# Kernel tuning notes

Measured on AMD Instinct MI355X. Metric: run time of the kernel, lower is better.

The kernel has to match this reference:

```python
import jax, jax.numpy as jnp
import numpy as np

N, FEATS, CLASSES, E = 100000, 32, 16, 1600000
EMB_DIM = 1 + int(np.log2(FEATS))  # 6
HIDDEN = 3 + EMB_DIM               # 9
DEPTH = 10
DIFF = 0.9


def setup_inputs() -> dict:
    key = jax.random.key(0)
    ks = jax.random.split(key, 10)
    s = lambda k, *sh: jax.random.normal(k, sh, dtype=jnp.float32)
    return {
        "x": s(ks[0], N, FEATS),
        "edges": jax.random.randint(ks[1], (2, E), 0, N, dtype=jnp.int64),
        "emb_table": s(ks[2], FEATS, EMB_DIM) * 0.1,
        "W1": s(ks[3], 1 + EMB_DIM, HIDDEN) * 0.3,
        "b1": jnp.zeros((HIDDEN,), jnp.float32),
        "W2": s(ks[4], HIDDEN, 1) * 0.3,
        "b2": jnp.zeros((1,), jnp.float32),
        "Wout": s(ks[5], FEATS, CLASSES) * 0.1,
        "bout": jnp.zeros((CLASSES,), jnp.float32),
    }


def reference(x, edges, emb_table, W1, b1, W2, b2, Wout, bout):
    n, f = x.shape
    src, dst = edges[0], edges[1]
    # symmetric degree normalization (parameter-free GraphConv)
    deg = jax.ops.segment_sum(jnp.ones((src.shape[0],), x.dtype), dst, num_segments=n)
    deg = jnp.maximum(deg, 1.0)
    norm = jax.lax.rsqrt(deg[src] * deg[dst])  # [E]

    def conv(h):
        return jax.ops.segment_sum(h[src] * norm[:, None], dst, num_segments=n)

    def diffuse(h):
        h0 = h
        for _ in range(DEPTH):
            h = conv(h) * DIFF + (1.0 - DIFF) * h0
        return h

    x = diffuse(x)
    # per-(node, class) MLP: x.t().reshape(-1,1) orders rows class-major
    col = x.T.reshape(-1, 1)                       # [f*n, 1]
    emb = jnp.repeat(emb_table, n, axis=0)         # [f*n, EMB_DIM] (class cl repeated n times)
    h = jnp.concatenate([col, emb], axis=1)        # [f*n, 1+EMB_DIM]
    h = jax.nn.relu(h @ W1 + b1)
    h = h @ W2 + b2                                # [f*n, 1]
    x = h.reshape(f, n).T                          # [n, f]
    x = diffuse(x)
    return x @ Wout + bout
```

## Files before the change

kernel.cpp:

```cpp
#include <hip/hip_runtime.h>
#include <hip/hip_fp16.h>

#define ELL_CAP 64
#define NSLICE 8
#define EPB 2048


__global__ __launch_bounds__(256) void ell_fill(
    const int* __restrict__ edges, int* __restrict__ deg,
    int* __restrict__ ell, int e, int n, int slice_sz) {
    int slice = blockIdx.x & (NSLICE - 1);
    int chunk = blockIdx.x >> 3;
    int lo = slice * slice_sz;
    int hi = min(n, lo + slice_sz);
    int base = chunk * EPB + threadIdx.x;
    int d[EPB / 256], s[EPB / 256];
#pragma unroll
    for (int k = 0; k < EPB / 256; ++k) {
        int i = base + k * 256;
        int valid = i < e;
        int ii = valid ? i : 0;
        int dv = edges[e + ii];
        int sv = edges[ii];
        d[k] = valid ? dv : -1;
        s[k] = sv;
    }
#pragma unroll
    for (int k = 0; k < EPB / 256; ++k) {
        int dv = d[k];
        if (dv < lo || dv >= hi) continue;
        int slot = atomicAdd(&deg[dv], 1);
        if (slot < ELL_CAP) ell[((size_t)dv << 6) + slot] = s[k];
    }
}

__global__ void nodeconst_kernel(const int* __restrict__ deg, float* __restrict__ rs,
                                 float* __restrict__ sq, float* __restrict__ wdeg,
                                 int* __restrict__ ell, int n) {
    int i = blockIdx.x * blockDim.x + threadIdx.x;
    if (i > n) return;
    int v = (i < n) ? deg[i] : 0;
    float d = (float)max(v, 1);
    float r = rsqrtf(d);
    rs[i] = r;
    sq[i] = sqrtf(d);
    wdeg[i] = 0.9f * r * r;
    if (i < n) {
        int dg = min(v, ELL_CAP);
        int dgp = (dg + 7) & ~7;
        for (int k = dg; k < dgp; ++k) ell[((size_t)i << 6) + k] = n;
    }
}

__global__ void prescale_kernel(const float2* __restrict__ x2, const float* __restrict__ rs,
                                __half2* __restrict__ g, int n) {
    int i = blockIdx.x * blockDim.x + threadIdx.x;
    int node = i >> 4;
    if (node > n) return;
    if (node == n) { g[i] = __floats2half2_rn(0.f, 0.f); return; }
    float2 v = x2[i];
    float r = rs[node];
    g[i] = __floats2half2_rn(v.x * r, v.y * r);
}


union H4 {
    uint2 u;
    __half2 h[2];
};

__device__ __forceinline__ void issue8(H4 (&P)[8], int idx, const uint2* __restrict__ gin, int q) {
    int t[8];
#pragma unroll
    for (int l = 0; l < 8; ++l) t[l] = __shfl(idx, l, 8);
#pragma unroll
    for (int l = 0; l < 8; ++l) P[l].u = gin[(size_t)t[l] * 8 + q];
}

__device__ __forceinline__ void accum8(H4 (&P)[8], __half2& b0l, __half2& b0h,
                                       __half2& b1l, __half2& b1h,
                                       __half2& b2l, __half2& b2h,
                                       __half2& b3l, __half2& b3h) {
    b0l = __hadd2(b0l, P[0].h[0]); b0h = __hadd2(b0h, P[0].h[1]);
    b1l = __hadd2(b1l, P[1].h[0]); b1h = __hadd2(b1h, P[1].h[1]);
    b2l = __hadd2(b2l, P[2].h[0]); b2h = __hadd2(b2h, P[2].h[1]);
    b3l = __hadd2(b3l, P[3].h[0]); b3h = __hadd2(b3h, P[3].h[1]);
    b0l = __hadd2(b0l, P[4].h[0]); b0h = __hadd2(b0h, P[4].h[1]);
    b1l = __hadd2(b1l, P[5].h[0]); b1h = __hadd2(b1h, P[5].h[1]);
    b2l = __hadd2(b2l, P[6].h[0]); b2h = __hadd2(b2h, P[6].h[1]);
    b3l = __hadd2(b3l, P[7].h[0]); b3h = __hadd2(b3h, P[7].h[1]);
}

__global__ __launch_bounds__(256) void conv_kernel(
    const uint2* __restrict__ gin, const uint2* __restrict__ g0,
    uint2* __restrict__ gout, const int* __restrict__ deg,
    const int* __restrict__ ell, const float* __restrict__ wdeg, int n) {
    int gid = blockIdx.x * blockDim.x + threadIdx.x;
    int node = gid >> 3;
    int q = gid & 7;
    if (node > n) return;
    int dg = (node < n) ? min(deg[node], ELL_CAP) : 0;
    int trips = (dg + 7) >> 3;
    int j0 = node << 6;
    float w = wdeg[node];
    H4 g0v;
    g0v.u = g0[gid];
    float ax = 0.f, ay = 0.f, az = 0.f, aw = 0.f;
    __half2 b0l = __floats2half2_rn(0.f, 0.f), b0h = b0l;
    __half2 b1l = b0l, b1h = b0l;
    __half2 b2l = b0l, b2h = b0l;
    __half2 b3l = b0l, b3h = b0l;

    auto ldidx = [&](int r) -> int {
        int v = ell[j0 + (min(r, 7) << 3) + q];
        return (r < trips) ? v : n;
    };

    if (trips > 0) {
        H4 A[8], B[8];
        int ia = ldidx(0);
        int ib = ldidx(1);
        issue8(A, ia, gin, q);
        issue8(B, ib, gin, q);
        int iters = (trips + 1) >> 1;
        for (int t = 0; t < iters; ++t) {
            int na = ldidx(2 * t + 2);
            int nb = ldidx(2 * t + 3);
            accum8(A, b0l, b0h, b1l, b1h, b2l, b2h, b3l, b3h);
            issue8(A, na, gin, q);
            accum8(B, b0l, b0h, b1l, b1h, b2l, b2h, b3l, b3h);
            issue8(B, nb, gin, q);
            {
                float2 ft;
                ft = __half22float2(b0l); ax += ft.x; ay += ft.y;
                ft = __half22float2(b0h); az += ft.x; aw += ft.y;
                ft = __half22float2(b1l); ax += ft.x; ay += ft.y;
                ft = __half22float2(b1h); az += ft.x; aw += ft.y;
                ft = __half22float2(b2l); ax += ft.x; ay += ft.y;
                ft = __half22float2(b2h); az += ft.x; aw += ft.y;
                ft = __half22float2(b3l); ax += ft.x; ay += ft.y;
                ft = __half22float2(b3h); az += ft.x; aw += ft.y;
                b0l = __floats2half2_rn(0.f, 0.f); b0h = b0l;
                b1l = b0l; b1h = b0l;
                b2l = b0l; b2h = b0l;
                b3l = b0l; b3h = b0l;
            }
        }
    }

    float2 g0lo = __half22float2(g0v.h[0]);
    float2 g0hi = __half22float2(g0v.h[1]);
    float rx = w * ax + 0.1f * g0lo.x;
    float ry = w * ay + 0.1f * g0lo.y;
    float rz = w * az + 0.1f * g0hi.x;
    float rw = w * aw + 0.1f * g0hi.y;
    H4 o;
    o.h[0] = __floats2half2_rn(rx, ry);
    o.h[1] = __floats2half2_rn(rz, rw);
    gout[gid] = o.u;
}


__global__ __launch_bounds__(256) void mlp_kernel(
    const __half* __restrict__ gin, __half* __restrict__ gout,
    const float* __restrict__ rs, const float* __restrict__ sq,
    const float* __restrict__ emb,
    const float* __restrict__ W1,
    const float* __restrict__ b1,
    const float* __restrict__ W2,
    const float* __restrict__ b2,
    int n) {
    __shared__ float c[32][9];
    __shared__ float w0[9], w2[9];
    __shared__ float b2s;
    int tid = threadIdx.x;
    for (int i = tid; i < 288; i += blockDim.x) {
        int f = i / 9, jj = i % 9;
        float acc = b1[jj];
#pragma unroll
        for (int k = 0; k < 6; ++k) acc += emb[f * 6 + k] * W1[(1 + k) * 9 + jj];
        c[f][jj] = acc;
    }
    if (tid < 9) { w0[tid] = W1[tid]; w2[tid] = W2[tid]; }
    if (tid == 0) b2s = b2[0];
    __syncthreads();
    int gid = blockIdx.x * blockDim.x + tid;
    int node = gid >> 5;
    if (node > n) return;
    if (node == n) { gout[gid] = __float2half_rn(0.f); return; }
    int f = gid & 31;
    float xv = __half2float(gin[gid]) * sq[node];
    float acc = b2s;
#pragma unroll
    for (int jj = 0; jj < 9; ++jj)
        acc += fmaxf(xv * w0[jj] + c[f][jj], 0.0f) * w2[jj];
    gout[gid] = __float2half_rn(acc * rs[node]);
}


__global__ __launch_bounds__(256) void out_kernel(
    const __half* __restrict__ g, const float* __restrict__ sq,
    const float* __restrict__ Wout, const float* __restrict__ bout,
    float* __restrict__ out, int n) {
    __shared__ float w[32 * 16];
    __shared__ float bo[16];
    int tid = threadIdx.x;
    for (int i = tid; i < 512; i += blockDim.x) w[i] = Wout[i];
    if (tid < 16) bo[tid] = bout[tid];
    __syncthreads();
    int gid = blockIdx.x * blockDim.x + tid;
    int node = gid >> 4;
    int cls = gid & 15;
    if (node >= n) return;
    const __half* gr = g + (size_t)node * 32;
    float acc = 0.0f;
#pragma unroll
    for (int f = 0; f < 32; ++f) acc += __half2float(gr[f]) * w[f * 16 + cls];
    out[gid] = acc * sq[node] + bo[cls];
}

extern "C" void kernel_launch(void* const* d_in, const int* in_sizes, int n_in,
                              void* d_out, int out_size, void* d_ws, size_t ws_size,
                              hipStream_t stream) {
    const float* x    = (const float*)d_in[0];
    const int* edges  = (const int*)d_in[1];
    const float* emb  = (const float*)d_in[2];
    const float* W1   = (const float*)d_in[3];
    const float* b1   = (const float*)d_in[4];
    const float* W2   = (const float*)d_in[5];
    const float* b2   = (const float*)d_in[6];
    const float* Wout = (const float*)d_in[7];
    const float* bout = (const float*)d_in[8];
    float* out        = (float*)d_out;

    const int N = in_sizes[0] / 32;
    const int E = in_sizes[1] / 2;

    size_t off = 0;
    auto walloc = [&](size_t bytes) {
        void* p = (char*)d_ws + off;
        off += (bytes + 255) & ~(size_t)255;
        return p;
    };
    int*     deg   = (int*)    walloc((size_t)(N + 1) * 4);
    float*   rs    = (float*)  walloc((size_t)(N + 1) * 4);
    float*   sq    = (float*)  walloc((size_t)(N + 1) * 4);
    float*   wdeg  = (float*)  walloc((size_t)(N + 1) * 4);
    int*     ell   = (int*)    walloc((size_t)(N + 1) * ELL_CAP * 4 + 256);
    __half*  g0buf = (__half*) walloc((size_t)(N + 1) * 32 * 2);
    __half*  bufA  = (__half*) walloc((size_t)(N + 1) * 32 * 2);
    __half*  bufB  = (__half*) walloc((size_t)(N + 1) * 32 * 2);

    hipMemsetAsync(deg, 0, (size_t)(N + 1) * 4, stream);
    {
        int slice_sz = (N + NSLICE - 1) / NSLICE;
        int chunks = (E + EPB - 1) / EPB;
        ell_fill<<<chunks * NSLICE, 256, 0, stream>>>(edges, deg, ell, E, N, slice_sz);
    }
    nodeconst_kernel<<<(N + 1 + 255) / 256, 256, 0, stream>>>(deg, rs, sq, wdeg, ell, N);

    const int conv_blocks = ((N + 1) * 8 + 255) / 256;
    const int elem_blocks = ((N + 1) * 32 + 255) / 256;
    const int pair_blocks = ((N + 1) * 16 + 255) / 256;

    prescale_kernel<<<pair_blocks, 256, 0, stream>>>((const float2*)x, rs,
                                                     (__half2*)g0buf, N);

    {
        const uint2* gin = (const uint2*)g0buf;
        for (int it = 0; it < 10; ++it) {
            uint2* go = (uint2*)((it & 1) ? bufB : bufA);
            conv_kernel<<<conv_blocks, 256, 0, stream>>>(gin, (const uint2*)g0buf, go,
                                                         deg, ell, wdeg, N);
            gin = go;
        }
    }
    mlp_kernel<<<elem_blocks, 256, 0, stream>>>(bufB, g0buf, rs, sq, emb, W1, b1, W2, b2, N);

    {
        const uint2* gin = (const uint2*)g0buf;
        for (int it = 0; it < 10; ++it) {
            uint2* go = (uint2*)((it & 1) ? bufB : bufA);
            conv_kernel<<<conv_blocks, 256, 0, stream>>>(gin, (const uint2*)g0buf, go,
                                                         deg, ell, wdeg, N);
            gin = go;
        }
    }
    out_kernel<<<(N * 16 + 255) / 256, 256, 0, stream>>>(bufB, sq, Wout, bout, out, N);
}
```

Measured before the change: 618.7 us.

## Split feature buffers into two 16-channel halves and run conv per half

Stores the 32-feature fp16 node state as two separate 16-feature planes and launches the ELL gather conv twice per diffusion step, once per plane, with 4 lanes per node. Each plane is half as large, so the gathered working set is more likely to stay resident in L2/MALL during the random neighbor gathers. The cost is twice the kernel launches, reading the ELL index lists twice, and narrower per-node gathers.

Result: slower. 829.3 us (+34.1%).

```diff
diff --git a/kernel.cpp b/kernel.cpp
--- a/kernel.cpp
+++ b/kernel.cpp
@@ -53,14 +53,21 @@
 }
 
 __global__ void prescale_kernel(const float2* __restrict__ x2, const float* __restrict__ rs,
-                                __half2* __restrict__ g, int n) {
+                                __half2* __restrict__ glo, __half2* __restrict__ ghi, int n) {
     int i = blockIdx.x * blockDim.x + threadIdx.x;
     int node = i >> 4;
     if (node > n) return;
-    if (node == n) { g[i] = __floats2half2_rn(0.f, 0.f); return; }
-    float2 v = x2[i];
-    float r = rs[node];
-    g[i] = __floats2half2_rn(v.x * r, v.y * r);
+    int p = i & 15;
+    __half2 v;
+    if (node == n) {
+        v = __floats2half2_rn(0.f, 0.f);
+    } else {
+        float2 t = x2[i];
+        float r = rs[node];
+        v = __floats2half2_rn(t.x * r, t.y * r);
+    }
+    if (p < 8) glo[(size_t)node * 8 + p] = v;
+    else       ghi[(size_t)node * 8 + (p - 8)] = v;
 }
 
 
@@ -69,12 +76,13 @@
     __half2 h[2];
 };
 
-__device__ __forceinline__ void issue8(H4 (&P)[8], int idx, const uint2* __restrict__ gin, int q) {
-    int t[8];
-#pragma unroll
-    for (int l = 0; l < 8; ++l) t[l] = __shfl(idx, l, 8);
-#pragma unroll
-    for (int l = 0; l < 8; ++l) P[l].u = gin[(size_t)t[l] * 8 + q];
+__device__ __forceinline__ void issue8h(H4 (&P)[8], int i0, int i1,
+                                        const uint2* __restrict__ gin, int q) {
+#pragma unroll
+    for (int j = 0; j < 8; ++j) {
+        int s = __shfl((j & 1) ? i1 : i0, j >> 1, 4);
+        P[j].u = gin[(size_t)s * 4 + q];
+    }
 }
 
 __device__ __forceinline__ void accum8(H4 (&P)[8], __half2& b0l, __half2& b0h,
@@ -91,13 +99,13 @@
     b3l = __hadd2(b3l, P[7].h[0]); b3h = __hadd2(b3h, P[7].h[1]);
 }
 
-__global__ __launch_bounds__(256) void conv_kernel(
+__global__ __launch_bounds__(256) void conv_half(
     const uint2* __restrict__ gin, const uint2* __restrict__ g0,
     uint2* __restrict__ gout, const int* __restrict__ deg,
     const int* __restrict__ ell, const float* __restrict__ wdeg, int n) {
     int gid = blockIdx.x * blockDim.x + threadIdx.x;
-    int node = gid >> 3;
-    int q = gid & 7;
+    int node = gid >> 2;
+    int q = gid & 3;
     if (node > n) return;
     int dg = (node < n) ? min(deg[node], ELL_CAP) : 0;
     int trips = (dg + 7) >> 3;
@@ -111,25 +119,30 @@
     __half2 b2l = b0l, b2h = b0l;
     __half2 b3l = b0l, b3h = b0l;
 
-    auto ldidx = [&](int r) -> int {
-        int v = ell[j0 + (min(r, 7) << 3) + q];
-        return (r < trips) ? v : n;
+    auto ldidx2 = [&](int r, int& i0, int& i1) {
+        int rr = min(r, 7);
+        int v0 = ell[j0 + (rr << 3) + 2 * q];
+        int v1 = ell[j0 + (rr << 3) + 2 * q + 1];
+        i0 = (r < trips) ? v0 : n;
+        i1 = (r < trips) ? v1 : n;
     };
 
     if (trips > 0) {
         H4 A[8], B[8];
-        int ia = ldidx(0);
-        int ib = ldidx(1);
-        issue8(A, ia, gin, q);
-        issue8(B, ib, gin, q);
+        int ia0, ia1, ib0, ib1;
+        ldidx2(0, ia0, ia1);
+        ldidx2(1, ib0, ib1);
+        issue8h(A, ia0, ia1, gin, q);
+        issue8h(B, ib0, ib1, gin, q);
         int iters = (trips + 1) >> 1;
         for (int t = 0; t < iters; ++t) {
-            int na = ldidx(2 * t + 2);
-            int nb = ldidx(2 * t + 3);
+            int na0, na1, nb0, nb1;
+            ldidx2(2 * t + 2, na0, na1);
+            ldidx2(2 * t + 3, nb0, nb1);
             accum8(A, b0l, b0h, b1l, b1h, b2l, b2h, b3l, b3h);
-            issue8(A, na, gin, q);
+            issue8h(A, na0, na1, gin, q);
             accum8(B, b0l, b0h, b1l, b1h, b2l, b2h, b3l, b3h);
-            issue8(B, nb, gin, q);
+            issue8h(B, nb0, nb1, gin, q);
             {
                 float2 ft;
                 ft = __half22float2(b0l); ax += ft.x; ay += ft.y;
@@ -162,7 +175,8 @@
 
 
 __global__ __launch_bounds__(256) void mlp_kernel(
-    const __half* __restrict__ gin, __half* __restrict__ gout,
+    const __half* __restrict__ ginlo, const __half* __restrict__ ginhi,
+    __half* __restrict__ goutlo, __half* __restrict__ gouthi,
     const float* __restrict__ rs, const float* __restrict__ sq,
     const float* __restrict__ emb,
     const float* __restrict__ W1,
@@ -187,19 +201,23 @@
     int gid = blockIdx.x * blockDim.x + tid;
     int node = gid >> 5;
     if (node > n) return;
-    if (node == n) { gout[gid] = __float2half_rn(0.f); return; }
     int f = gid & 31;
-    float xv = __half2float(gin[gid]) * sq[node];
+    size_t half_idx = (size_t)node * 16 + (f & 15);
+    __half* dst = (f < 16) ? (goutlo + half_idx) : (gouthi + half_idx);
+    if (node == n) { *dst = __float2half_rn(0.f); return; }
+    const __half* src = (f < 16) ? (ginlo + half_idx) : (ginhi + half_idx);
+    float xv = __half2float(*src) * sq[node];
     float acc = b2s;
 #pragma unroll
     for (int jj = 0; jj < 9; ++jj)
         acc += fmaxf(xv * w0[jj] + c[f][jj], 0.0f) * w2[jj];
-    gout[gid] = __float2half_rn(acc * rs[node]);
+    *dst = __float2half_rn(acc * rs[node]);
 }
 
 
 __global__ __launch_bounds__(256) void out_kernel(
-    const __half* __restrict__ g, const float* __restrict__ sq,
+    const __half* __restrict__ glo, const __half* __restrict__ ghi,
+    const float* __restrict__ sq,
     const float* __restrict__ Wout, const float* __restrict__ bout,
     float* __restrict__ out, int n) {
     __shared__ float w[32 * 16];
@@ -212,10 +230,13 @@
     int node = gid >> 4;
     int cls = gid & 15;
     if (node >= n) return;
-    const __half* gr = g + (size_t)node * 32;
+    const __half* glo_r = glo + (size_t)node * 16;
+    const __half* ghi_r = ghi + (size_t)node * 16;
     float acc = 0.0f;
 #pragma unroll
-    for (int f = 0; f < 32; ++f) acc += __half2float(gr[f]) * w[f * 16 + cls];
+    for (int f = 0; f < 16; ++f) acc += __half2float(glo_r[f]) * w[f * 16 + cls];
+#pragma unroll
+    for (int f = 0; f < 16; ++f) acc += __half2float(ghi_r[f]) * w[(16 + f) * 16 + cls];
     out[gid] = acc * sq[node] + bo[cls];
 }
 
@@ -242,14 +263,18 @@
         off += (bytes + 255) & ~(size_t)255;
         return p;
     };
+    const size_t halfb = (size_t)(N + 1) * 16 * 2;
     int*     deg   = (int*)    walloc((size_t)(N + 1) * 4);
     float*   rs    = (float*)  walloc((size_t)(N + 1) * 4);
     float*   sq    = (float*)  walloc((size_t)(N + 1) * 4);
     float*   wdeg  = (float*)  walloc((size_t)(N + 1) * 4);
     int*     ell   = (int*)    walloc((size_t)(N + 1) * ELL_CAP * 4 + 256);
-    __half*  g0buf = (__half*) walloc((size_t)(N + 1) * 32 * 2);
-    __half*  bufA  = (__half*) walloc((size_t)(N + 1) * 32 * 2);
-    __half*  bufB  = (__half*) walloc((size_t)(N + 1) * 32 * 2);
+    __half*  g0lo  = (__half*) walloc(halfb);
+    __half*  g0hi  = (__half*) walloc(halfb);
+    __half*  Alo   = (__half*) walloc(halfb);
+    __half*  Ahi   = (__half*) walloc(halfb);
+    __half*  Blo   = (__half*) walloc(halfb);
+    __half*  Bhi   = (__half*) walloc(halfb);
 
     hipMemsetAsync(deg, 0, (size_t)(N + 1) * 4, stream);
     {
@@ -259,32 +284,38 @@
     }
     nodeconst_kernel<<<(N + 1 + 255) / 256, 256, 0, stream>>>(deg, rs, sq, wdeg, ell, N);
 
-    const int conv_blocks = ((N + 1) * 8 + 255) / 256;
-    const int elem_blocks = ((N + 1) * 32 + 255) / 256;
-    const int pair_blocks = ((N + 1) * 16 + 255) / 256;
+    const int convh_blocks = ((N + 1) * 4 + 255) / 256;
+    const int elem_blocks  = ((N + 1) * 32 + 255) / 256;
+    const int pair_blocks  = ((N + 1) * 16 + 255) / 256;
 
     prescale_kernel<<<pair_blocks, 256, 0, stream>>>((const float2*)x, rs,
-                                                     (__half2*)g0buf, N);
+                                                     (__half2*)g0lo, (__half2*)g0hi, N);
 
     {
-        const uint2* gin = (const uint2*)g0buf;
+        const __half *gilo = g0lo, *gihi = g0hi;
         for (int it = 0; it < 10; ++it) {
-            uint2* go = (uint2*)((it & 1) ? bufB : bufA);
-            conv_kernel<<<conv_blocks, 256, 0, stream>>>(gin, (const uint2*)g0buf, go,
-                                                         deg, ell, wdeg, N);
-            gin = go;
+            __half* golo = (it & 1) ? Blo : Alo;
+            __half* gohi = (it & 1) ? Bhi : Ahi;
+            conv_half<<<convh_blocks, 256, 0, stream>>>(
+                (const uint2*)gilo, (const uint2*)g0lo, (uint2*)golo, deg, ell, wdeg, N);
+            conv_half<<<convh_blocks, 256, 0, stream>>>(
+                (const uint2*)gihi, (const uint2*)g0hi, (uint2*)gohi, deg, ell, wdeg, N);
+            gilo = golo; gihi = gohi;
         }
     }
-    mlp_kernel<<<elem_blocks, 256, 0, stream>>>(bufB, g0buf, rs, sq, emb, W1, b1, W2, b2, N);
-
+    mlp_kernel<<<elem_blocks, 256, 0, stream>>>(Blo, Bhi, g0lo, g0hi,
+                                                rs, sq, emb, W1, b1, W2, b2, N);
     {
-        const uint2* gin = (const uint2*)g0buf;
+        const __half *gilo = g0lo, *gihi = g0hi;
         for (int it = 0; it < 10; ++it) {
-            uint2* go = (uint2*)((it & 1) ? bufB : bufA);
-            conv_kernel<<<conv_blocks, 256, 0, stream>>>(gin, (const uint2*)g0buf, go,
-                                                         deg, ell, wdeg, N);
-            gin = go;
+            __half* golo = (it & 1) ? Blo : Alo;
+            __half* gohi = (it & 1) ? Bhi : Ahi;
+            conv_half<<<convh_blocks, 256, 0, stream>>>(
+                (const uint2*)gilo, (const uint2*)g0lo, (uint2*)golo, deg, ell, wdeg, N);
+            conv_half<<<convh_blocks, 256, 0, stream>>>(
+                (const uint2*)gihi, (const uint2*)g0hi, (uint2*)gohi, deg, ell, wdeg, N);
+            gilo = golo; gihi = gohi;
         }
     }
-    out_kernel<<<(N * 16 + 255) / 256, 256, 0, stream>>>(bufB, sq, Wout, bout, out, N);
-}
+    out_kernel<<<(N * 16 + 255) / 256, 256, 0, stream>>>(Blo, Bhi, sq, Wout, bout, out, N);
+}
```

## Fuse final diffusion step into MLP and output-projection kernels; nontemporal conv stores

Applied to the files above, without the earlier changes.

The last conv iteration of each diffusion pass is folded into the following per-node MLP kernel and the final Wout projection kernel. A shared conv_core device function serves all three variants. The output projection now reduces the 16 class sums across the 8 lanes of each node with xor shuffles. This removes two launches and a round trip of a half-precision node buffer through memory. Conv outputs are also written with nontemporal stores, which could hurt cache reuse because the next iteration reads those buffers right away.

After: 602.8 us. -2.6%, faster.

```diff
diff --git a/kernel.cpp b/kernel.cpp
--- a/kernel.cpp
+++ b/kernel.cpp
@@ -66,6 +66,7 @@
 
 union H4 {
     uint2 u;
+    unsigned long long ull;
     __half2 h[2];
 };
 
@@ -91,14 +92,11 @@
     b3l = __hadd2(b3l, P[7].h[0]); b3h = __hadd2(b3h, P[7].h[1]);
 }
 
-__global__ __launch_bounds__(256) void conv_kernel(
+__device__ __forceinline__ float4 conv_core(
+    int node, int q, int gid,
     const uint2* __restrict__ gin, const uint2* __restrict__ g0,
-    uint2* __restrict__ gout, const int* __restrict__ deg,
-    const int* __restrict__ ell, const float* __restrict__ wdeg, int n) {
-    int gid = blockIdx.x * blockDim.x + threadIdx.x;
-    int node = gid >> 3;
-    int q = gid & 7;
-    if (node > n) return;
+    const int* __restrict__ deg, const int* __restrict__ ell,
+    const float* __restrict__ wdeg, int n) {
     int dg = (node < n) ? min(deg[node], ELL_CAP) : 0;
     int trips = (dg + 7) >> 3;
     int j0 = node << 6;
@@ -150,31 +148,38 @@
 
     float2 g0lo = __half22float2(g0v.h[0]);
     float2 g0hi = __half22float2(g0v.h[1]);
-    float rx = w * ax + 0.1f * g0lo.x;
-    float ry = w * ay + 0.1f * g0lo.y;
-    float rz = w * az + 0.1f * g0hi.x;
-    float rw = w * aw + 0.1f * g0hi.y;
+    return make_float4(w * ax + 0.1f * g0lo.x, w * ay + 0.1f * g0lo.y,
+                       w * az + 0.1f * g0hi.x, w * aw + 0.1f * g0hi.y);
+}
+
+__global__ __launch_bounds__(256) void conv_kernel(
+    const uint2* __restrict__ gin, const uint2* __restrict__ g0,
+    uint2* __restrict__ gout, const int* __restrict__ deg,
+    const int* __restrict__ ell, const float* __restrict__ wdeg, int n) {
+    int gid = blockIdx.x * blockDim.x + threadIdx.x;
+    int node = gid >> 3;
+    int q = gid & 7;
+    if (node > n) return;
+    float4 r = conv_core(node, q, gid, gin, g0, deg, ell, wdeg, n);
     H4 o;
-    o.h[0] = __floats2half2_rn(rx, ry);
-    o.h[1] = __floats2half2_rn(rz, rw);
-    gout[gid] = o.u;
-}
-
-
-__global__ __launch_bounds__(256) void mlp_kernel(
-    const __half* __restrict__ gin, __half* __restrict__ gout,
+    o.h[0] = __floats2half2_rn(r.x, r.y);
+    o.h[1] = __floats2half2_rn(r.z, r.w);
+    __builtin_nontemporal_store(o.ull, reinterpret_cast<unsigned long long*>(gout) + gid);
+}
+
+__global__ __launch_bounds__(256) void conv_mlp_kernel(
+    const uint2* __restrict__ gin, const uint2* __restrict__ g0,
+    uint2* __restrict__ gout, const int* __restrict__ deg,
+    const int* __restrict__ ell, const float* __restrict__ wdeg,
     const float* __restrict__ rs, const float* __restrict__ sq,
-    const float* __restrict__ emb,
-    const float* __restrict__ W1,
-    const float* __restrict__ b1,
-    const float* __restrict__ W2,
-    const float* __restrict__ b2,
-    int n) {
+    const float* __restrict__ emb, const float* __restrict__ W1,
+    const float* __restrict__ b1, const float* __restrict__ W2,
+    const float* __restrict__ b2, int n) {
     __shared__ float c[32][9];
     __shared__ float w0[9], w2[9];
     __shared__ float b2s;
     int tid = threadIdx.x;
-    for (int i = tid; i < 288; i += blockDim.x) {
+    for (int i = tid; i < 288; i += 256) {
         int f = i / 9, jj = i % 9;
         float acc = b1[jj];
 #pragma unroll
@@ -185,38 +190,63 @@
     if (tid == 0) b2s = b2[0];
     __syncthreads();
     int gid = blockIdx.x * blockDim.x + tid;
-    int node = gid >> 5;
+    int node = gid >> 3;
+    int q = gid & 7;
     if (node > n) return;
-    if (node == n) { gout[gid] = __float2half_rn(0.f); return; }
-    int f = gid & 31;
-    float xv = __half2float(gin[gid]) * sq[node];
-    float acc = b2s;
-#pragma unroll
-    for (int jj = 0; jj < 9; ++jj)
-        acc += fmaxf(xv * w0[jj] + c[f][jj], 0.0f) * w2[jj];
-    gout[gid] = __float2half_rn(acc * rs[node]);
-}
-
-
-__global__ __launch_bounds__(256) void out_kernel(
-    const __half* __restrict__ g, const float* __restrict__ sq,
+    H4 o;
+    if (node == n) {
+        o.h[0] = __floats2half2_rn(0.f, 0.f);
+        o.h[1] = o.h[0];
+    } else {
+        float4 r = conv_core(node, q, gid, gin, g0, deg, ell, wdeg, n);
+        float vals[4] = {r.x, r.y, r.z, r.w};
+        float s = sq[node], rr = rs[node];
+#pragma unroll
+        for (int j = 0; j < 4; ++j) {
+            int f = 4 * q + j;
+            float xv = vals[j] * s;
+            float acc = b2s;
+#pragma unroll
+            for (int jj = 0; jj < 9; ++jj)
+                acc += fmaxf(xv * w0[jj] + c[f][jj], 0.0f) * w2[jj];
+            vals[j] = acc * rr;
+        }
+        o.h[0] = __floats2half2_rn(vals[0], vals[1]);
+        o.h[1] = __floats2half2_rn(vals[2], vals[3]);
+    }
+    gout[gid] = o.u;
+}
+
+__global__ __launch_bounds__(256) void conv_out_kernel(
+    const uint2* __restrict__ gin, const uint2* __restrict__ g0,
+    const int* __restrict__ deg, const int* __restrict__ ell,
+    const float* __restrict__ wdeg, const float* __restrict__ sq,
     const float* __restrict__ Wout, const float* __restrict__ bout,
     float* __restrict__ out, int n) {
     __shared__ float w[32 * 16];
     __shared__ float bo[16];
     int tid = threadIdx.x;
-    for (int i = tid; i < 512; i += blockDim.x) w[i] = Wout[i];
+    for (int i = tid; i < 512; i += 256) w[i] = Wout[i];
     if (tid < 16) bo[tid] = bout[tid];
     __syncthreads();
     int gid = blockIdx.x * blockDim.x + tid;
-    int node = gid >> 4;
-    int cls = gid & 15;
+    int node = gid >> 3;
+    int q = gid & 7;
     if (node >= n) return;
-    const __half* gr = g + (size_t)node * 32;
-    float acc = 0.0f;
-#pragma unroll
-    for (int f = 0; f < 32; ++f) acc += __half2float(gr[f]) * w[f * 16 + cls];
-    out[gid] = acc * sq[node] + bo[cls];
+    float4 r = conv_core(node, q, gid, gin, g0, deg, ell, wdeg, n);
+    float s = sq[node];
+    float v0 = r.x * s, v1 = r.y * s, v2 = r.z * s, v3 = r.w * s;
+    const float* w4 = w + 4 * q * 16;
+    float cls[16];
+#pragma unroll
+    for (int k = 0; k < 16; ++k)
+        cls[k] = v0 * w4[k] + v1 * w4[16 + k] + v2 * w4[32 + k] + v3 * w4[48 + k];
+#pragma unroll
+    for (int m = 1; m < 8; m <<= 1)
+#pragma unroll
+        for (int k = 0; k < 16; ++k) cls[k] += __shfl_xor(cls[k], m, 8);
+    out[(size_t)node * 16 + 2 * q]     = cls[2 * q]     + bo[2 * q];
+    out[(size_t)node * 16 + 2 * q + 1] = cls[2 * q + 1] + bo[2 * q + 1];
 }
 
 extern "C" void kernel_launch(void* const* d_in, const int* in_sizes, int n_in,
@@ -260,7 +290,6 @@
     nodeconst_kernel<<<(N + 1 + 255) / 256, 256, 0, stream>>>(deg, rs, sq, wdeg, ell, N);
 
     const int conv_blocks = ((N + 1) * 8 + 255) / 256;
-    const int elem_blocks = ((N + 1) * 32 + 255) / 256;
     const int pair_blocks = ((N + 1) * 16 + 255) / 256;
 
     prescale_kernel<<<pair_blocks, 256, 0, stream>>>((const float2*)x, rs,
@@ -268,23 +297,25 @@
 
     {
         const uint2* gin = (const uint2*)g0buf;
-        for (int it = 0; it < 10; ++it) {
+        for (int it = 0; it < 9; ++it) {
             uint2* go = (uint2*)((it & 1) ? bufB : bufA);
             conv_kernel<<<conv_blocks, 256, 0, stream>>>(gin, (const uint2*)g0buf, go,
                                                          deg, ell, wdeg, N);
             gin = go;
         }
-    }
-    mlp_kernel<<<elem_blocks, 256, 0, stream>>>(bufB, g0buf, rs, sq, emb, W1, b1, W2, b2, N);
-
+        conv_mlp_kernel<<<conv_blocks, 256, 0, stream>>>(
+            gin, (const uint2*)g0buf, (uint2*)g0buf, deg, ell, wdeg,
+            rs, sq, emb, W1, b1, W2, b2, N);
+    }
     {
         const uint2* gin = (const uint2*)g0buf;
-        for (int it = 0; it < 10; ++it) {
+        for (int it = 0; it < 9; ++it) {
             uint2* go = (uint2*)((it & 1) ? bufB : bufA);
             conv_kernel<<<conv_blocks, 256, 0, stream>>>(gin, (const uint2*)g0buf, go,
                                                          deg, ell, wdeg, N);
             gin = go;
         }
-    }
-    out_kernel<<<(N * 16 + 255) / 256, 256, 0, stream>>>(bufB, sq, Wout, bout, out, N);
-}
+        conv_out_kernel<<<conv_blocks, 256, 0, stream>>>(
+            gin, (const uint2*)g0buf, deg, ell, wdeg, sq, Wout, bout, out, N);
+    }
+}
```
